# Kernel optimization log

Hardware: AMD Instinct MI355X
Metric: run time of the kernel (lower is better)

The kernel has to match this reference:

```python
import jax, jax.numpy as jnp
import numpy as np

X_GRID, Y_GRID = 192, 132
HW = X_GRID * Y_GRID            # 25344
NUM_PROP = 500
NUM_CLS = 6
RADIUS = 10
L_WIN = (2 * RADIUS + 1) ** 2   # 441
D = 128
N_HEADS = 8
D_HEAD = D // N_HEADS
VX, VY = 0.64, 0.64             # feature_map_stride * voxel_size
PC_X0, PC_Y0 = -61.44, -42.24


def _bev_pos():
    # create_2D_grid: linspace(0, size-1, size) + 0.5, meshgrid 'ij', flatten row-major
    bx, by = jnp.meshgrid(jnp.arange(X_GRID, dtype=jnp.float32) + 0.5,
                          jnp.arange(Y_GRID, dtype=jnp.float32) + 0.5, indexing='ij')
    return jnp.stack([bx.reshape(-1), by.reshape(-1)], axis=-1)[None]  # [1, HW, 2]


def conv2d(x, w, b):
    y = jax.lax.conv_general_dilated(x, w, (1, 1), 'SAME',
                                     dimension_numbers=('NCHW', 'OIHW', 'NCHW'))
    return y + b[None, :, None, None]


def maxpool3_valid(x):
    return jax.lax.reduce_window(x, -jnp.inf, jax.lax.max,
                                 (1, 1, 3, 3), (1, 1, 1, 1), 'VALID')


def layer_norm(x, g, b, eps=1e-5):
    m = jnp.mean(x, axis=-1, keepdims=True)
    v = jnp.var(x, axis=-1, keepdims=True)
    return (x - m) * jax.lax.rsqrt(v + eps) * g + b


def pos_emb(p, W1, b1, W2, b2):
    return jax.nn.relu(p @ W1 + b1) @ W2 + b2


def _forward(inputs, W_shared, b_shared, W_hm, b_hm, W_cls, b_cls,
             W_pos1, b_pos1, W_pos2, b_pos2, Wq, bq, Wk, bk, Wv, bv, Wo, bo,
             ln1_g, ln1_b, ln2_g, ln2_b, W_ff1, b_ff1, W_ff2, b_ff2,
             W_center, b_center, W_height, b_height, W_dim, b_dim,
             W_rot, b_rot, W_iou, b_iou, W_hm2, b_hm2):
    x = jnp.transpose(inputs, (0, 1, 3, 2))          # [B,C,192,132]
    B = x.shape[0]
    lidar_feat = jax.nn.relu(conv2d(x, W_shared, b_shared))   # [B,128,192,132]
    lff = lidar_feat.reshape(B, D, HW)

    dense_heatmap = conv2d(lidar_feat, W_hm, b_hm)            # [B,6,192,132]
    heatmap = jax.nn.sigmoid(jax.lax.stop_gradient(dense_heatmap))  # detached in original

    # local-max NMS: 3x3 maxpool on inner region, zeros at border; classes 3..5 bypass NMS
    inner = maxpool3_valid(heatmap)
    local_max = jnp.pad(inner, ((0, 0), (0, 0), (1, 1), (1, 1)))
    local_max = local_max.at[:, 3:6].set(heatmap[:, 3:6])
    hm = heatmap * (heatmap == local_max)

    # threshold + top-k proposals (replaces nonzero+pad+MySortImpe plugin)
    hm_flat = hm.reshape(B, NUM_CLS * HW)
    vals = jnp.where(hm_flat > 0.01, hm_flat, 0.0)
    _, top = jax.lax.top_k(vals, NUM_PROP)            # [B,500]
    cls = top // HW
    sp = top % HW

    query_feat = jnp.take_along_axis(lff, sp[:, None, :], axis=2)  # [B,128,500]
    oh = jax.nn.one_hot(cls, NUM_CLS, dtype=lff.dtype)             # [B,500,6]
    query_feat = query_feat + jnp.einsum('bpc,oc->bop', oh, W_cls) + b_cls[None, :, None]

    bev_pos = jnp.broadcast_to(_bev_pos(), (B, HW, 2))
    query_pos = jnp.take_along_axis(bev_pos, sp[:, :, None], axis=1)  # [B,500,2]

    # windowed key indices (faithful to original //x_grid, %y_grid arithmetic)
    rng = jnp.arange(-RADIUS, RADIUS + 1)
    rx, ry = jnp.meshgrid(rng, rng, indexing='ij')
    kx = (sp // X_GRID)[:, :, None, None] + rx[None, None]
    ky = (sp % Y_GRID)[:, :, None, None] + ry[None, None]
    key_idx = kx.reshape(B, NUM_PROP, L_WIN) * X_GRID + ky.reshape(B, NUM_PROP, L_WIN)
    key_mask = (key_idx < 0) | (key_idx >= HW)
    key_idx = jnp.clip(key_idx, 0, HW - 1)

    key_feat = jnp.take_along_axis(lff, key_idx.reshape(B, 1, -1), axis=2)
    key_feat = key_feat.reshape(B, D, NUM_PROP, L_WIN)
    key_pos = jnp.take_along_axis(bev_pos, key_idx.reshape(B, -1, 1), axis=1)
    key_pos = key_pos.reshape(B, NUM_PROP, L_WIN, 2)

    # decoder: cross-attention of each proposal over its 441-key window
    N = B * NUM_PROP
    q = query_feat.transpose(0, 2, 1).reshape(N, D)
    k = key_feat.transpose(0, 2, 3, 1).reshape(N, L_WIN, D)
    mask = key_mask.reshape(N, L_WIN)
    qpe = pos_emb(query_pos.reshape(N, 2), W_pos1, b_pos1, W_pos2, b_pos2)
    kpe = pos_emb(key_pos.reshape(N, L_WIN, 2), W_pos1, b_pos1, W_pos2, b_pos2)

    qh = ((q + qpe) @ Wq + bq).reshape(N, N_HEADS, D_HEAD)
    kh = ((k + kpe) @ Wk + bk).reshape(N, L_WIN, N_HEADS, D_HEAD)
    vh = (k @ Wv + bv).reshape(N, L_WIN, N_HEADS, D_HEAD)
    scores = jnp.einsum('nhd,nlhd->nhl', qh, kh) / np.float32(np.sqrt(D_HEAD))
    scores = jnp.where(mask[:, None, :], jnp.float32(-1e9), scores)
    attn = jax.nn.softmax(scores, axis=-1)
    ctx = jnp.einsum('nhl,nlhd->nhd', attn, vh).reshape(N, D)
    x1 = layer_norm(q + ctx @ Wo + bo, ln1_g, ln1_b)
    ff = jax.nn.relu(x1 @ W_ff1 + b_ff1) @ W_ff2 + b_ff2
    x2 = layer_norm(x1 + ff, ln2_g, ln2_b)

    qf = x2.reshape(B, NUM_PROP, D).transpose(0, 2, 1)   # [B,128,500]
    head = lambda W, b: jnp.einsum('bcp,oc->bop', qf, W) + b[None, :, None]
    center = head(W_center, b_center) + query_pos.transpose(0, 2, 1)
    height = head(W_height, b_height)
    dim = head(W_dim, b_dim)
    rot = head(W_rot, b_rot)
    iou = head(W_iou, b_iou)
    hm2 = head(W_hm2, b_hm2)

    # get_bboxes / decode_bbox
    score = jax.nn.sigmoid(hm2)                          # [B,6,500]
    _ = (iou + 1.0) * 0.5                                # computed, unused (as in original)
    final_preds = jnp.argmax(score, axis=1).astype(score.dtype)
    final_scores = jnp.max(score, axis=1)
    cx = center[:, 0:1] * VX + PC_X0
    cy = center[:, 1:2] * VY + PC_Y0
    dim = jnp.exp(dim)
    height = height - dim[:, 2:3] * 0.5
    rot = jnp.arctan(rot[:, 0:1] / (rot[:, 1:2] + 1e-6))
    box = jnp.concatenate([cx, cy, height, dim, rot,
                           final_preds[:, None, :], final_scores[:, None, :]], axis=1)
    return box.transpose(0, 2, 1)                        # [B,500,9]


def setup_inputs() -> dict:
    key = jax.random.key(0)
    ks = jax.random.split(key, 20)
    r = lambda k, shape, s=0.02: jax.random.normal(k, shape, dtype=jnp.float32) * s
    z = lambda n: jnp.zeros((n,), dtype=jnp.float32)
    o = lambda n: jnp.ones((n,), dtype=jnp.float32)
    return {
        'inputs': jax.random.normal(ks[0], (1, 256, 132, 192), dtype=jnp.float32),
        'W_shared': r(ks[1], (128, 256, 3, 3)), 'b_shared': z(128),
        'W_hm': r(ks[2], (6, 128, 3, 3)), 'b_hm': z(6),
        'W_cls': r(ks[3], (128, 6)), 'b_cls': z(128),
        'W_pos1': r(ks[4], (2, 128)), 'b_pos1': z(128),
        'W_pos2': r(ks[5], (128, 128)), 'b_pos2': z(128),
        'Wq': r(ks[6], (128, 128)), 'bq': z(128),
        'Wk': r(ks[7], (128, 128)), 'bk': z(128),
        'Wv': r(ks[8], (128, 128)), 'bv': z(128),
        'Wo': r(ks[9], (128, 128)), 'bo': z(128),
        'ln1_g': o(128), 'ln1_b': z(128),
        'ln2_g': o(128), 'ln2_b': z(128),
        'W_ff1': r(ks[10], (128, 256)), 'b_ff1': z(256),
        'W_ff2': r(ks[11], (256, 128)), 'b_ff2': z(128),
        'W_center': r(ks[12], (2, 128)), 'b_center': z(2),
        'W_height': r(ks[13], (1, 128)), 'b_height': z(1),
        'W_dim': r(ks[14], (3, 128)), 'b_dim': z(3),
        'W_rot': r(ks[15], (2, 128)), 'b_rot': z(2),
        'W_iou': r(ks[16], (1, 128)), 'b_iou': z(1),
        'W_hm2': r(ks[17], (6, 128)), 'b_hm2': z(6),
    }


def reference(inputs, W_shared, b_shared, W_hm, b_hm, W_cls, b_cls,
              W_pos1, b_pos1, W_pos2, b_pos2, Wq, bq, Wk, bk, Wv, bv, Wo, bo,
              ln1_g, ln1_b, ln2_g, ln2_b, W_ff1, b_ff1, W_ff2, b_ff2,
              W_center, b_center, W_height, b_height, W_dim, b_dim,
              W_rot, b_rot, W_iou, b_iou, W_hm2, b_hm2):
    return _forward(inputs, W_shared, b_shared, W_hm, b_hm, W_cls, b_cls,
                    W_pos1, b_pos1, W_pos2, b_pos2, Wq, bq, Wk, bk, Wv, bv, Wo, bo,
                    ln1_g, ln1_b, ln2_g, ln2_b, W_ff1, b_ff1, W_ff2, b_ff2,
                    W_center, b_center, W_height, b_height, W_dim, b_dim,
                    W_rot, b_rot, W_iou, b_iou, W_hm2, b_hm2)
```

## Files before the change

### kernel.cpp

```cpp
#include <hip/hip_runtime.h>
#include <math.h>
#include <float.h>

#define XG 192
#define YG 132
#define HW 25344
#define NCLS 6
#define NPROP 500
#define LWIN 441
#define CAP 2048

typedef unsigned short ushort_t;
typedef __attribute__((ext_vector_type(8))) short bf8v;
typedef __attribute__((ext_vector_type(4))) float f4v;

static __device__ __forceinline__ int imin(int a,int b){return a<b?a:b;}
static __device__ __forceinline__ int imax(int a,int b){return a>b?a:b;}

__device__ __forceinline__ void gl_lds16(const float* gp, float* lp){
  __builtin_amdgcn_global_load_lds(
      (const __attribute__((address_space(1))) unsigned int*)gp,
      (__attribute__((address_space(3))) unsigned int*)lp,
      16, 0, 0);
}
__device__ __forceinline__ void gl_lds16u(const ushort_t* gp, ushort_t* lp){
  __builtin_amdgcn_global_load_lds(
      (const __attribute__((address_space(1))) unsigned int*)gp,
      (__attribute__((address_space(3))) unsigned int*)lp,
      16, 0, 0);
}

__device__ __forceinline__ ushort_t f2bf(float x){
  unsigned u = __float_as_uint(x);
  return (ushort_t)((u + 0x7FFFu + ((u>>16)&1u)) >> 16);
}
__device__ __forceinline__ float bf2f(ushort_t h){
  return __uint_as_float(((unsigned)h)<<16);
}

__global__ __launch_bounds__(256) void k_wt(const float* __restrict__ Ws,
                                            const float* __restrict__ Whm,
                                            const float* __restrict__ Wq,
                                            const float* __restrict__ Wp2,
                                            const float* __restrict__ Wo,
                                            const float* __restrict__ Wf1,
                                            const float* __restrict__ Wf2,
                                            float* __restrict__ W6,
                                            float* __restrict__ WQT,
                                            float* __restrict__ WP2T,
                                            float* __restrict__ WOT,
                                            float* __restrict__ WF1T,
                                            float* __restrict__ WF2T,
                                            ushort_t* __restrict__ BQ0,
                                            ushort_t* __restrict__ BQ1,
                                            ushort_t* __restrict__ BQ2,
                                            int* __restrict__ Z){
  int t = blockIdx.x*256 + threadIdx.x;
  if (t < 294912){
    int kl = t & 31;
    int rest = t >> 5;
    int n = rest & 127;
    int tc = rest >> 7;
    int tap = tc >> 3, chunk = tc & 7;
    int c = chunk*32 + kl;
    float v = Ws[(size_t)n*2304 + c*9 + tap];
    ushort_t h0 = f2bf(v);
    float r1 = v - bf2f(h0);
    ushort_t h1 = f2bf(r1);
    float r2 = r1 - bf2f(h1);
    ushort_t h2 = f2bf(r2);
    size_t dst = (size_t)tc*5120 + n*40 + kl;
    BQ0[dst] = h0; BQ1[dst] = h1; BQ2[dst] = h2;
  }
  if (t < 6912){
    int c = t & 127, row = t >> 7;
    int cls = row / 9, tap = row % 9;
    W6[t] = Whm[(size_t)cls*1152 + c*9 + tap];
  }
  if (t < 16384){
    int k = t & 127, c = t >> 7;
    WQT[t]  = Wq [(size_t)k*128 + c];
    WP2T[t] = Wp2[(size_t)k*128 + c];
    WOT[t]  = Wo [(size_t)k*128 + c];
  }
  if (t < 32768){
    { int k = t & 127, o = t >> 7;  WF1T[t] = Wf1[(size_t)k*256 + o]; }
    { int k = t & 255, c = t >> 8;  WF2T[t] = Wf2[(size_t)k*128 + c]; }
  }
  if (t < 65568) Z[t] = 0;
}

__global__ __launch_bounds__(256, 3) void k_conv1(const float* __restrict__ IN,
                                                  const ushort_t* __restrict__ BQ0,
                                                  const ushort_t* __restrict__ BQ1,
                                                  const ushort_t* __restrict__ BQ2,
                                                  float* __restrict__ P0,
                                                  float* __restrict__ P1){
  const int b  = blockIdx.x;
  const int g  = blockIdx.y;
  const int i0 = (b % 3) * 64;
  const int j  = b / 3;
  const int tid = threadIdx.x;
  const int w    = tid >> 6;
  const int lane = tid & 63;
  const int l15  = lane & 15, quad = lane >> 4;
  __shared__ __align__(16) ushort_t SM[23280];
  ushort_t* As0 = SM;
  ushort_t* As1 = SM + 2640;
  ushort_t* As2 = SM + 5280;
  ushort_t* Bs0 = SM + 7920;
  ushort_t* Bs1 = SM + 13040;
  ushort_t* Bs2 = SM + 18160;
  f4v acc[4][2];
  #pragma unroll
  for (int mq=0;mq<4;++mq)
    #pragma unroll
    for (int nt=0;nt<2;++nt) acc[mq][nt] = (f4v){0.f,0.f,0.f,0.f};

  for (int cq=0; cq<4; ++cq){
    const int chunk = g*4 + cq;
    for (int kw=0; kw<3; ++kw){
      __syncthreads();
      {
        int gj = j - 1 + kw;
        bool jok = (unsigned)gj < 132u;
        for (int e = tid; e < 2112; e += 256){
          int c = e / 66, ii = e - c*66;
          int gi = i0 - 1 + ii;
          float v = 0.f;
          if (jok && (unsigned)gi < 192u)
            v = IN[(size_t)(chunk*32 + c)*25344 + gj*192 + gi];
          ushort_t h0 = f2bf(v);
          float r1 = v - bf2f(h0);
          ushort_t h1 = f2bf(r1);
          float r2 = r1 - bf2f(h1);
          ushort_t h2 = f2bf(r2);
          int a = ii*40 + c;
          As0[a] = h0; As1[a] = h1; As2[a] = h2;
        }
      }
      for (int kh=0; kh<3; ++kh){
        if (kh > 0) __syncthreads();
        {
          int tc = (kh*3 + kw)*8 + chunk;
          const ushort_t* s0 = BQ0 + (size_t)tc*5120;
          const ushort_t* s1 = BQ1 + (size_t)tc*5120;
          const ushort_t* s2 = BQ2 + (size_t)tc*5120;
          gl_lds16u(s0 + (size_t)tid*8,       Bs0 + (size_t)(w*64)*8);
          gl_lds16u(s0 + (size_t)(256+tid)*8, Bs0 + (size_t)(256 + w*64)*8);
          gl_lds16u(s1 + (size_t)tid*8,       Bs1 + (size_t)(w*64)*8);
          gl_lds16u(s1 + (size_t)(256+tid)*8, Bs1 + (size_t)(256 + w*64)*8);
          gl_lds16u(s2 + (size_t)tid*8,       Bs2 + (size_t)(w*64)*8);
          gl_lds16u(s2 + (size_t)(256+tid)*8, Bs2 + (size_t)(256 + w*64)*8);
          if (tid < 128){
            gl_lds16u(s0 + (size_t)(512+tid)*8, Bs0 + (size_t)(512 + w*64)*8);
            gl_lds16u(s1 + (size_t)(512+tid)*8, Bs1 + (size_t)(512 + w*64)*8);
            gl_lds16u(s2 + (size_t)(512+tid)*8, Bs2 + (size_t)(512 + w*64)*8);
          }
        }
        __syncthreads();
        bf8v A0[4], A1[4], A2[4];
        #pragma unroll
        for (int mq=0; mq<4; ++mq){
          int off = (mq*16 + l15 + kh)*40 + quad*8;
          A0[mq] = *(const bf8v*)&As0[off];
          A1[mq] = *(const bf8v*)&As1[off];
          A2[mq] = *(const bf8v*)&As2[off];
        }
        bf8v B0[2], B1[2], B2[2];
        #pragma unroll
        for (int ntl=0; ntl<2; ++ntl){
          int off = ((w*2+ntl)*16 + l15)*40 + quad*8;
          B0[ntl] = *(const bf8v*)&Bs0[off];
          B1[ntl] = *(const bf8v*)&Bs1[off];
          B2[ntl] = *(const bf8v*)&Bs2[off];
        }
        #pragma unroll
        for (int mq=0;mq<4;++mq){
          #pragma unroll
          for (int ntl=0;ntl<2;++ntl){
            f4v c = acc[mq][ntl];
            c = __builtin_amdgcn_mfma_f32_16x16x32_bf16(A0[mq], B0[ntl], c, 0,0,0);
            c = __builtin_amdgcn_mfma_f32_16x16x32_bf16(A0[mq], B1[ntl], c, 0,0,0);
            c = __builtin_amdgcn_mfma_f32_16x16x32_bf16(A1[mq], B0[ntl], c, 0,0,0);
            c = __builtin_amdgcn_mfma_f32_16x16x32_bf16(A0[mq], B2[ntl], c, 0,0,0);
            c = __builtin_amdgcn_mfma_f32_16x16x32_bf16(A1[mq], B1[ntl], c, 0,0,0);
            c = __builtin_amdgcn_mfma_f32_16x16x32_bf16(A2[mq], B0[ntl], c, 0,0,0);
            acc[mq][ntl] = c;
          }
        }
      }
    }
  }
  __syncthreads();
  float* Cs = (float*)SM;
  #pragma unroll
  for (int mq=0;mq<4;++mq)
    #pragma unroll
    for (int ntl=0;ntl<2;++ntl)
      #pragma unroll
      for (int r=0;r<4;++r){
        int m = mq*16 + quad*4 + r;
        int oc = (w*2+ntl)*16 + l15;
        Cs[m*128 + oc] = acc[mq][ntl][r];
      }
  __syncthreads();
  float* dst = g ? P1 : P0;
  for (int e = tid; e < 2048; e += 256){
    int m = e >> 5, ocq = e & 31;
    float4 v = *(float4*)&Cs[m*128 + ocq*4];
    int p = (i0 + m)*132 + j;
    *(float4*)&dst[(size_t)p*128 + ocq*4] = v;
  }
}

__global__ __launch_bounds__(256) void k_cadd2(float* __restrict__ LFF,
                                               const float* __restrict__ P0,
                                               const float* __restrict__ P1,
                                               const float* __restrict__ bias){
  int t = blockIdx.x*256 + threadIdx.x;
  float4 a = ((const float4*)P0)[t];
  float4 b = ((const float4*)P1)[t];
  float4 bs = ((const float4*)bias)[t & 31];
  float4 r;
  r.x = fmaxf(a.x+b.x+bs.x, 0.f);
  r.y = fmaxf(a.y+b.y+bs.y, 0.f);
  r.z = fmaxf(a.z+b.z+bs.z, 0.f);
  r.w = fmaxf(a.w+b.w+bs.w, 0.f);
  ((float4*)LFF)[t] = r;
}

__global__ __launch_bounds__(256) void k_mid(const float* __restrict__ LFF,
                                             const float* __restrict__ W1, const float* __restrict__ b1,
                                             const float* __restrict__ W2, const float* __restrict__ b2,
                                             const float* __restrict__ Wk, const float* __restrict__ bk,
                                             const float* __restrict__ Wv, const float* __restrict__ bv,
                                             float* __restrict__ KK, float* __restrict__ VV,
                                             const float* __restrict__ W6, const float* __restrict__ bhm,
                                             float* __restrict__ HMS){
  __shared__ float smem[12288];
  const int tid = threadIdx.x;
  const int wv4 = tid >> 6;
  if (blockIdx.x < 792){
    float* hs   = smem;
    float* sf   = smem + 4096;
    float* wbuf = smem + 8192;
    const int p0 = blockIdx.x*32;
    for (int e=tid; e<4096; e+=256){
      int k = e>>5, px = e&31;
      int p = p0+px;
      float bx = (float)(p/132)+0.5f, by = (float)(p%132)+0.5f;
      hs[k*32+px] = fmaxf(bx*W1[k] + by*W1[128+k] + b1[k], 0.f);
    }
    for (int e=tid; e<4096; e+=256){
      int px = e>>7, k = e&127;
      sf[k*32+px] = LFF[(size_t)(p0+px)*128 + k];
    }
    const int pxg = tid & 15, ocg = tid >> 4;
    const int px0 = pxg*2, oc0 = ocg*8;
    float accA[2][8];
    #pragma unroll
    for (int r=0;r<2;++r)
      #pragma unroll
      for (int u=0;u<8;++u) accA[r][u]=0.f;
    for (int c0=0; c0<128; c0+=32){
      __syncthreads();
      const float* wsrc = W2 + (size_t)c0*128;
      #pragma unroll
      for (int r=0;r<4;++r)
        gl_lds16(wsrc + (size_t)(r*256+tid)*4, wbuf + (size_t)(r*256+wv4*64)*4);
      __syncthreads();
      #pragma unroll 2
      for (int k=0;k<32;++k){
        float a0 = hs[(c0+k)*32+px0], a1 = hs[(c0+k)*32+px0+1];
        const float4* w = (const float4*)(wbuf + (size_t)k*128 + oc0);
        float4 w0 = w[0], w1 = w[1];
        accA[0][0]+=a0*w0.x; accA[0][1]+=a0*w0.y; accA[0][2]+=a0*w0.z; accA[0][3]+=a0*w0.w;
        accA[0][4]+=a0*w1.x; accA[0][5]+=a0*w1.y; accA[0][6]+=a0*w1.z; accA[0][7]+=a0*w1.w;
        accA[1][0]+=a1*w0.x; accA[1][1]+=a1*w0.y; accA[1][2]+=a1*w0.z; accA[1][3]+=a1*w0.w;
        accA[1][4]+=a1*w1.x; accA[1][5]+=a1*w1.y; accA[1][6]+=a1*w1.z; accA[1][7]+=a1*w1.w;
      }
    }
    __syncthreads();
    #pragma unroll
    for (int u=0;u<8;++u){
      float bb = b2[oc0+u];
      hs[(oc0+u)*32+px0]   = sf[(oc0+u)*32+px0]   + accA[0][u] + bb;
      hs[(oc0+u)*32+px0+1] = sf[(oc0+u)*32+px0+1] + accA[1][u] + bb;
    }
    float accK[2][8], accV[2][8];
    #pragma unroll
    for (int u=0;u<8;++u){
      float k0 = bk[oc0+u], v0 = bv[oc0+u];
      accK[0][u]=k0; accK[1][u]=k0; accV[0][u]=v0; accV[1][u]=v0;
    }
    for (int c0=0; c0<128; c0+=16){
      __syncthreads();
      #pragma unroll
      for (int r=0;r<2;++r){
        gl_lds16(Wk + (size_t)c0*128 + (size_t)(r*256+tid)*4, wbuf + (size_t)(r*256+wv4*64)*4);
        gl_lds16(Wv + (size_t)c0*128 + (size_t)(r*256+tid)*4, wbuf + 2048 + (size_t)(r*256+wv4*64)*4);
      }
      __syncthreads();
      #pragma unroll 2
      for (int k=0;k<16;++k){
        int kk = c0+k;
        float s0 = hs[kk*32+px0], s1 = hs[kk*32+px0+1];
        float f0 = sf[kk*32+px0], f1 = sf[kk*32+px0+1];
        const float4* wkp = (const float4*)(wbuf + (size_t)k*128 + oc0);
        const float4* wvp = (const float4*)(wbuf + 2048 + (size_t)k*128 + oc0);
        float4 k0v = wkp[0], k1v = wkp[1], v0v = wvp[0], v1v = wvp[1];
        accK[0][0]+=s0*k0v.x; accK[0][1]+=s0*k0v.y; accK[0][2]+=s0*k0v.z; accK[0][3]+=s0*k0v.w;
        accK[0][4]+=s0*k1v.x; accK[0][5]+=s0*k1v.y; accK[0][6]+=s0*k1v.z; accK[0][7]+=s0*k1v.w;
        accK[1][0]+=s1*k0v.x; accK[1][1]+=s1*k0v.y; accK[1][2]+=s1*k0v.z; accK[1][3]+=s1*k0v.w;
        accK[1][4]+=s1*k1v.x; accK[1][5]+=s1*k1v.y; accK[1][6]+=s1*k1v.z; accK[1][7]+=s1*k1v.w;
        accV[0][0]+=f0*v0v.x; accV[0][1]+=f0*v0v.y; accV[0][2]+=f0*v0v.z; accV[0][3]+=f0*v0v.w;
        accV[0][4]+=f0*v1v.x; accV[0][5]+=f0*v1v.y; accV[0][6]+=f0*v1v.z; accV[0][7]+=f0*v1v.w;
        accV[1][0]+=f1*v0v.x; accV[1][1]+=f1*v0v.y; accV[1][2]+=f1*v0v.z; accV[1][3]+=f1*v0v.w;
        accV[1][4]+=f1*v1v.x; accV[1][5]+=f1*v1v.y; accV[1][6]+=f1*v1v.z; accV[1][7]+=f1*v1v.w;
      }
    }
    #pragma unroll
    for (int r=0;r<2;++r){
      int p = p0+px0+r;
      float4* oK = (float4*)(KK + (size_t)p*128 + oc0);
      float4* oV = (float4*)(VV + (size_t)p*128 + oc0);
      float4 t0, t1;
      t0.x=accK[r][0]; t0.y=accK[r][1]; t0.z=accK[r][2]; t0.w=accK[r][3];
      t1.x=accK[r][4]; t1.y=accK[r][5]; t1.z=accK[r][6]; t1.w=accK[r][7];
      oK[0]=t0; oK[1]=t1;
      t0.x=accV[r][0]; t0.y=accV[r][1]; t0.z=accV[r][2]; t0.w=accV[r][3];
      t1.x=accV[r][4]; t1.y=accV[r][5]; t1.z=accV[r][6]; t1.w=accV[r][7];
      oV[0]=t0; oV[1]=t1;
    }
  } else {
    float* w6s = smem;
    float* red = smem + 8192;
    for (int e=tid; e<6912; e+=256) w6s[e] = W6[e];
    __syncthreads();
    int lane = tid & 63, wave = tid >> 6;
    int p = (blockIdx.x - 792)*64 + lane;
    int i = p/132, j = p%132;
    float acc[6] = {0.f,0.f,0.f,0.f,0.f,0.f};
    int cbase = wave*32;
    #pragma unroll
    for (int kh=0; kh<3; ++kh){
      int gi = i+kh-1;
      if ((unsigned)gi >= 192u) continue;
      #pragma unroll
      for (int kw=0; kw<3; ++kw){
        int gj = j+kw-1;
        if ((unsigned)gj >= 132u) continue;
        const float* row = LFF + (size_t)(gi*132+gj)*128 + cbase;
        int tap = kh*3+kw;
        #pragma unroll
        for (int cq=0; cq<8; ++cq){
          float4 v = *(const float4*)(row + cq*4);
          #pragma unroll
          for (int cls=0; cls<6; ++cls){
            float4 wv = *(const float4*)(w6s + (size_t)(cls*9+tap)*128 + cbase + cq*4);
            acc[cls] += v.x*wv.x + v.y*wv.y + v.z*wv.z + v.w*wv.w;
          }
        }
      }
    }
    __syncthreads();
    #pragma unroll
    for (int c=0;c<6;++c) red[(wave*6+c)*64 + lane] = acc[c];
    __syncthreads();
    if (wave==0){
      #pragma unroll
      for (int c=0;c<6;++c){
        float s = red[c*64+lane] + red[(6+c)*64+lane] + red[(12+c)*64+lane] + red[(18+c)*64+lane] + bhm[c];
        HMS[(size_t)c*HW + p] = 1.f/(1.f+expf(-s));
      }
    }
  }
}

__global__ __launch_bounds__(256) void k_nms(const float* __restrict__ HMS,
                                             float* __restrict__ VALS,
                                             int* __restrict__ HIST){
  int t = blockIdx.x*256 + threadIdx.x;
  int c = t / HW, p = t % HW;
  int i = p/132, j = p%132;
  float h = HMS[t];
  float v;
  if (c < 3){
    v = 0.f;
    if (i>=1 && i<=190 && j>=1 && j<=130){
      float m = -1e30f;
      #pragma unroll
      for (int di=-1;di<=1;++di)
        #pragma unroll
        for (int dj=-1;dj<=1;++dj)
          m = fmaxf(m, HMS[(size_t)c*HW + (i+di)*132 + (j+dj)]);
      if (h == m) v = h;
    }
  } else v = h;
  if (!(v > 0.01f)) v = 0.f;
  VALS[t] = v;
  if (v > 0.f) atomicAdd(HIST + (__float_as_uint(v)>>16), 1);
}

__global__ __launch_bounds__(1024) void k_scan(const int* __restrict__ HIST, int* __restrict__ SCAN){
  __shared__ int part[1024];
  __shared__ int gsel;
  int t = threadIdx.x;
  int s = 0, base = t*64;
  for (int u=0;u<64;++u) s += HIST[base+u];
  part[t] = s;
  __syncthreads();
  for (int off=1; off<1024; off<<=1){
    int add = (t+off < 1024) ? part[t+off] : 0;
    __syncthreads();
    part[t] += add;
    __syncthreads();
  }
  int total = part[0];
  int mineI = part[t];
  int nextI = (t < 1023) ? part[t+1] : 0;
  if (mineI >= NPROP && nextI < NPROP) gsel = t;
  if (t == 0 && total < NPROP) gsel = -1;
  __syncthreads();
  int g = gsel;
  if (g < 0){
    if (t==0){ SCAN[0] = 0; SCAN[1] = total; }
    return;
  }
  int cumG = (g < 1023) ? part[g+1] : 0;
  if (t < 64){
    int x = HIST[g*64 + t];
    #pragma unroll
    for (int off=1; off<64; off<<=1){
      int y = __shfl_down(x, off);
      x += (t + off < 64) ? y : 0;
    }
    int Snext = __shfl_down(x, 1);
    int incl  = cumG + x;
    int nextc = (t==63) ? cumG : cumG + Snext;
    if (incl >= NPROP && nextc < NPROP){
      SCAN[0] = g*64 + t;
      SCAN[1] = nextc;
    }
  }
}

__global__ __launch_bounds__(256) void k_collect(const float* __restrict__ VALS,
                                                 const int* __restrict__ SCAN,
                                                 int* __restrict__ CNT,
                                                 float* __restrict__ CV, int* __restrict__ CI){
  int t = blockIdx.x*256 + threadIdx.x;
  float v = VALS[t];
  int bstar = SCAN[0];
  if (v > 0.f && (int)(__float_as_uint(v)>>16) >= bstar){
    int pos = atomicAdd(CNT, 1);
    if (pos < CAP){ CV[pos] = v; CI[pos] = t; }
  }
}

__global__ __launch_bounds__(1024) void k_sort(const float* __restrict__ CV, const int* __restrict__ CI,
                                               const int* __restrict__ CNT,
                                               int* __restrict__ TOPS, int* __restrict__ TOPC){
  __shared__ float sv[CAP];
  __shared__ int   si[CAP];
  int tid = threadIdx.x;
  int M = imin(CNT[0], CAP);
  for (int i=tid; i<CAP; i+=1024){
    if (i < M){ sv[i] = CV[i]; si[i] = CI[i]; }
    else      { sv[i] = -1.f;  si[i] = 0x7fffffff; }
  }
  __syncthreads();
  for (int k=2; k<=CAP; k<<=1){
    for (int j=k>>1; j>0; j>>=1){
      for (int i=tid; i<CAP; i+=1024){
        int p = i ^ j;
        if (p > i){
          bool up = ((i & k) == 0);
          float va = sv[i], vb = sv[p];
          int ia = si[i], ib = si[p];
          bool aFirst = (va > vb) || (va == vb && ia < ib);
          bool bFirst = (vb > va) || (vb == va && ib < ia);
          bool doswap = up ? bFirst : aFirst;
          if (doswap){ sv[i]=vb; sv[p]=va; si[i]=ib; si[p]=ia; }
        }
      }
      __syncthreads();
    }
  }
  for (int t=tid; t<NPROP; t+=1024){
    int idx = imin(si[t], NCLS*HW - 1);
    TOPC[t] = idx / HW;
    TOPS[t] = idx % HW;
  }
}

__global__ __launch_bounds__(256) void k_attn(const float* __restrict__ KK, const float* __restrict__ VV,
                                              const float* __restrict__ LFF,
                                              const int* __restrict__ TOPS, const int* __restrict__ TOPC,
                                              const float* __restrict__ Wcls, const float* __restrict__ bcls,
                                              const float* __restrict__ pW1, const float* __restrict__ pb1,
                                              const float* __restrict__ WP2T, const float* __restrict__ pb2,
                                              const float* __restrict__ WQT, const float* __restrict__ bq,
                                              const float* __restrict__ WOT, const float* __restrict__ bo,
                                              const float* __restrict__ g1, const float* __restrict__ b1,
                                              const float* __restrict__ WF1T, const float* __restrict__ bf1,
                                              const float* __restrict__ WF2T, const float* __restrict__ bf2,
                                              const float* __restrict__ g2, const float* __restrict__ b2,
                                              const float* __restrict__ Wc, const float* __restrict__ bc,
                                              const float* __restrict__ Wh, const float* __restrict__ bh,
                                              const float* __restrict__ Wd, const float* __restrict__ bd,
                                              const float* __restrict__ Wr, const float* __restrict__ br,
                                              const float* __restrict__ Whm2, const float* __restrict__ bhm2,
                                              float* __restrict__ out){
  int n = blockIdx.x, tid = threadIdx.x;
  __shared__ __align__(16) float qhL[128];
  __shared__ float sc[8*441];
  __shared__ int   kiL[441];
  __shared__ __align__(16) float ctxL[128];
  __shared__ float xL[128];
  __shared__ float hidL[256];
  __shared__ float sumsL[8];
  __shared__ float stat[2];
  __shared__ float dots[16];
  int sp = TOPS[n];
  int cls = TOPC[n];
  const int kb64 = (tid>>7)*64, c128 = tid&127;
  float qreg = 0.f;
  if (tid < 128){
    float qx = (float)(sp/132)+0.5f, qy = (float)(sp%132)+0.5f;
    ctxL[tid] = fmaxf(qx*pW1[tid] + qy*pW1[128+tid] + pb1[tid], 0.f);
    qreg = LFF[(size_t)sp*128+tid] + Wcls[tid*6+cls] + bcls[tid];
  }
  __syncthreads();
  {
    const float4* wp = (const float4*)(WP2T + (size_t)c128*128 + kb64);
    float pe = 0.f;
    #pragma unroll
    for (int k4=0;k4<16;++k4){
      float4 w = wp[k4]; int kb = kb64 + k4*4;
      pe += ctxL[kb]*w.x + ctxL[kb+1]*w.y + ctxL[kb+2]*w.z + ctxL[kb+3]*w.w;
    }
    sc[tid] = pe;
  }
  __syncthreads();
  if (tid < 128) xL[tid] = qreg + pb2[tid] + sc[tid] + sc[tid+128];
  __syncthreads();
  {
    const float4* wp = (const float4*)(WQT + (size_t)c128*128 + kb64);
    float qh = 0.f;
    #pragma unroll
    for (int k4=0;k4<16;++k4){
      float4 w = wp[k4]; int kb = kb64 + k4*4;
      qh += xL[kb]*w.x + xL[kb+1]*w.y + xL[kb+2]*w.z + xL[kb+3]*w.w;
    }
    sc[tid] = qh;
  }
  __syncthreads();
  if (tid < 128) qhL[tid] = bq[tid] + sc[tid] + sc[tid+128];
  __syncthreads();
  int spx = sp/192, spy = sp%132;
  for (int l = tid; l < 441; l += 256){
    int a = l/21, bb = l%21;
    int kidx = (spx + a - 10)*192 + (spy + bb - 10);
    bool msk = (kidx < 0) || (kidx >= HW);
    int kc = imin(imax(kidx,0), HW-1);
    kiL[l] = kc;
    const float4* kk4 = (const float4*)(KK + (size_t)kc*128);
    const float4* qh4 = (const float4*)qhL;
    #pragma unroll
    for (int hh=0; hh<8; ++hh){
      float acc = 0.f;
      #pragma unroll
      for (int d4=0; d4<4; ++d4){
        float4 kv = kk4[hh*4+d4]; float4 qv = qh4[hh*4+d4];
        acc += kv.x*qv.x + kv.y*qv.y + kv.z*qv.z + kv.w*qv.w;
      }
      sc[hh*441+l] = msk ? -1e9f : acc*0.25f;
    }
  }
  __syncthreads();
  int wave = tid>>6, lane = tid&63;
  for (int hh = wave; hh < 8; hh += 4){
    float mx = -3.0e38f;
    for (int l = lane; l < 441; l += 64) mx = fmaxf(mx, sc[hh*441+l]);
    #pragma unroll
    for (int off=32; off; off>>=1) mx = fmaxf(mx, __shfl_xor(mx, off));
    float sum = 0.f;
    for (int l = lane; l < 441; l += 64){
      float e = __expf(sc[hh*441+l] - mx);
      sc[hh*441+l] = e; sum += e;
    }
    #pragma unroll
    for (int off=32; off; off>>=1) sum += __shfl_xor(sum, off);
    if (lane==0) sumsL[hh] = sum;
  }
  __syncthreads();
  for (int hh = wave; hh < 8; hh += 4){
    float a[16];
    #pragma unroll
    for (int d=0; d<16; ++d) a[d]=0.f;
    for (int l = lane; l < 441; l += 64){
      float w = sc[hh*441+l];
      const float4* vv4 = (const float4*)(VV + (size_t)kiL[l]*128 + hh*16);
      #pragma unroll
      for (int d4=0; d4<4; ++d4){
        float4 v = vv4[d4];
        a[d4*4+0]+=w*v.x; a[d4*4+1]+=w*v.y; a[d4*4+2]+=w*v.z; a[d4*4+3]+=w*v.w;
      }
    }
    #pragma unroll
    for (int d=0; d<16; ++d){
      #pragma unroll
      for (int off=32; off; off>>=1) a[d] += __shfl_xor(a[d], off);
    }
    if (lane==0){
      float inv = 1.f/sumsL[hh];
      #pragma unroll
      for (int d=0; d<16; ++d) ctxL[hh*16+d] = a[d]*inv;
    }
  }
  __syncthreads();
  {
    const float4* wp = (const float4*)(WOT + (size_t)c128*128 + kb64);
    float acc = 0.f;
    #pragma unroll
    for (int k4=0;k4<16;++k4){
      float4 w = wp[k4]; int kb = kb64 + k4*4;
      acc += ctxL[kb]*w.x + ctxL[kb+1]*w.y + ctxL[kb+2]*w.z + ctxL[kb+3]*w.w;
    }
    sc[tid] = acc;
  }
  __syncthreads();
  float x1v = 0.f;
  if (tid < 128){
    x1v = qreg + bo[tid] + sc[tid] + sc[tid+128];
    xL[tid] = x1v;
  }
  __syncthreads();
  if (tid < 64){
    float u0 = xL[tid], u1 = xL[tid+64];
    float s = u0+u1, s2 = u0*u0+u1*u1;
    #pragma unroll
    for (int off=32; off; off>>=1){ s += __shfl_xor(s, off); s2 += __shfl_xor(s2, off); }
    if (tid==0){ float mean = s*(1.f/128.f); float var = s2*(1.f/128.f) - mean*mean;
      stat[0]=mean; stat[1]=rsqrtf(var + 1e-5f); }
  }
  __syncthreads();
  if (tid < 128) xL[tid] = (x1v - stat[0])*stat[1]*g1[tid] + b1[tid];
  __syncthreads();
  {
    const float4* wp = (const float4*)(WF1T + (size_t)tid*128);
    float hv = bf1[tid];
    #pragma unroll 8
    for (int k4=0;k4<32;++k4){
      float4 w = wp[k4]; int kb = k4*4;
      hv += xL[kb]*w.x + xL[kb+1]*w.y + xL[kb+2]*w.z + xL[kb+3]*w.w;
    }
    hidL[tid] = fmaxf(hv, 0.f);
  }
  __syncthreads();
  {
    int kb0 = (tid>>7)*128;
    const float4* wp = (const float4*)(WF2T + (size_t)c128*256 + kb0);
    float acc = 0.f;
    #pragma unroll 8
    for (int k4=0;k4<32;++k4){
      float4 w = wp[k4]; int kb = kb0 + k4*4;
      acc += hidL[kb]*w.x + hidL[kb+1]*w.y + hidL[kb+2]*w.z + hidL[kb+3]*w.w;
    }
    sc[tid] = acc;
  }
  __syncthreads();
  float x2v = 0.f;
  if (tid < 128) x2v = xL[tid] + bf2[tid] + sc[tid] + sc[tid+128];
  __syncthreads();
  if (tid < 128) hidL[tid] = x2v;
  __syncthreads();
  if (tid < 64){
    float u0 = hidL[tid], u1 = hidL[tid+64];
    float s = u0+u1, s2 = u0*u0+u1*u1;
    #pragma unroll
    for (int off=32; off; off>>=1){ s += __shfl_xor(s, off); s2 += __shfl_xor(s2, off); }
    if (tid==0){ float mean = s*(1.f/128.f); float var = s2*(1.f/128.f) - mean*mean;
      stat[0]=mean; stat[1]=rsqrtf(var + 1e-5f); }
  }
  __syncthreads();
  if (tid < 128) xL[tid] = (x2v - stat[0])*stat[1]*g2[tid] + b2[tid];
  __syncthreads();
  if (tid < 14){
    const float* Wp; float bb;
    if (tid < 2)      { Wp = Wc + tid*128;        bb = bc[tid];      }
    else if (tid < 3) { Wp = Wh;                  bb = bh[0];        }
    else if (tid < 6) { Wp = Wd + (tid-3)*128;    bb = bd[tid-3];    }
    else if (tid < 8) { Wp = Wr + (tid-6)*128;    bb = br[tid-6];    }
    else              { Wp = Whm2 + (tid-8)*128;  bb = bhm2[tid-8];  }
    float acc = bb;
    for (int k=0;k<128;++k) acc += xL[k]*Wp[k];
    dots[tid] = acc;
  }
  __syncthreads();
  if (tid == 0){
    float qpx = (float)(sp/132)+0.5f, qpy = (float)(sp%132)+0.5f;
    float cx = (dots[0]+qpx)*0.64f - 61.44f;
    float cy = (dots[1]+qpy)*0.64f - 42.24f;
    float e0 = expf(dots[3]), e1 = expf(dots[4]), e2 = expf(dots[5]);
    float hgt = dots[2] - e2*0.5f;
    float rot = atanf(dots[6]/(dots[7] + 1e-6f));
    float bestv = -1.f; int bestc = 0;
    #pragma unroll
    for (int m=0;m<6;++m){
      float s = 1.f/(1.f + expf(-dots[8+m]));
      if (s > bestv){ bestv = s; bestc = m; }
    }
    float* o = out + (size_t)n*9;
    o[0]=cx; o[1]=cy; o[2]=hgt; o[3]=e0; o[4]=e1; o[5]=e2; o[6]=rot;
    o[7]=(float)bestc; o[8]=bestv;
  }
}

extern "C" void kernel_launch(void* const* d_in, const int* in_sizes, int n_in,
                              void* d_out, int out_size, void* d_ws, size_t ws_size,
                              hipStream_t stream){
  (void)in_sizes; (void)n_in; (void)out_size;
  const float* IN   = (const float*)d_in[0];
  const float* Wsh  = (const float*)d_in[1];
  const float* bsh  = (const float*)d_in[2];
  const float* Whm  = (const float*)d_in[3];
  const float* bhm  = (const float*)d_in[4];
  const float* Wcls = (const float*)d_in[5];
  const float* bcls = (const float*)d_in[6];
  const float* Wp1  = (const float*)d_in[7];
  const float* bp1  = (const float*)d_in[8];
  const float* Wp2  = (const float*)d_in[9];
  const float* bp2  = (const float*)d_in[10];
  const float* Wq   = (const float*)d_in[11];
  const float* bq   = (const float*)d_in[12];
  const float* Wk   = (const float*)d_in[13];
  const float* bk   = (const float*)d_in[14];
  const float* Wv   = (const float*)d_in[15];
  const float* bv   = (const float*)d_in[16];
  const float* Wo   = (const float*)d_in[17];
  const float* bo   = (const float*)d_in[18];
  const float* g1   = (const float*)d_in[19];
  const float* b1   = (const float*)d_in[20];
  const float* g2   = (const float*)d_in[21];
  const float* b2   = (const float*)d_in[22];
  const float* Wf1  = (const float*)d_in[23];
  const float* bf1  = (const float*)d_in[24];
  const float* Wf2  = (const float*)d_in[25];
  const float* bf2  = (const float*)d_in[26];
  const float* Wc   = (const float*)d_in[27];
  const float* bc   = (const float*)d_in[28];
  const float* Wh   = (const float*)d_in[29];
  const float* bh   = (const float*)d_in[30];
  const float* Wd   = (const float*)d_in[31];
  const float* bd   = (const float*)d_in[32];
  const float* Wr   = (const float*)d_in[33];
  const float* br   = (const float*)d_in[34];
  const float* Whm2 = (const float*)d_in[37];
  const float* bhm2 = (const float*)d_in[38];
  float* out = (float*)d_out;
  float* W = (float*)d_ws;

  const size_t N_LFF  = (size_t)HW*128;
  const size_t OFF_LFF  = 0;
  const size_t OFF_KK   = OFF_LFF + N_LFF;
  const size_t OFF_VV   = OFF_KK + N_LFF;
  const size_t OFF_W6   = OFF_VV + N_LFF;
  const size_t OFF_HMS  = OFF_W6 + 6912;
  const size_t OFF_VALS = OFF_HMS + 152064;
  const size_t OFF_HIST = OFF_VALS + 152064;
  const size_t OFF_SCAN = OFF_HIST + 65536;
  const size_t OFF_CNT  = OFF_SCAN + 16;
  const size_t OFF_CV   = OFF_CNT + 16;
  const size_t OFF_CI   = OFF_CV + CAP;
  const size_t OFF_TOPS = OFF_CI + CAP;
  const size_t OFF_TOPC = OFF_TOPS + 512;
  const size_t OFF_WQT  = OFF_TOPC + 512;
  const size_t OFF_WP2T = OFF_WQT + 16384;
  const size_t OFF_WOT  = OFF_WP2T + 16384;
  const size_t OFF_WF1T = OFF_WOT + 16384;
  const size_t OFF_WF2T = OFF_WF1T + 32768;
  const size_t OFF_BQ0  = OFF_WF2T + 32768;
  const size_t OFF_BQ1  = OFF_BQ0 + 184320;
  const size_t OFF_BQ2  = OFF_BQ1 + 184320;
  const size_t TOTAL    = OFF_BQ2 + 184320;
  if (ws_size < TOTAL*sizeof(float)) return;

  ushort_t* BQ0 = (ushort_t*)(W + OFF_BQ0);
  ushort_t* BQ1 = (ushort_t*)(W + OFF_BQ1);
  ushort_t* BQ2 = (ushort_t*)(W + OFF_BQ2);

  k_wt    <<<1152, 256, 0, stream>>>(Wsh, Whm, Wq, Wp2, Wo, Wf1, Wf2,
                                     W+OFF_W6,
                                     W+OFF_WQT, W+OFF_WP2T, W+OFF_WOT, W+OFF_WF1T, W+OFF_WF2T,
                                     BQ0, BQ1, BQ2,
                                     (int*)(W+OFF_HIST));
  k_conv1 <<<dim3(396,2), 256, 0, stream>>>(IN, BQ0, BQ1, BQ2, W+OFF_KK, W+OFF_VV);
  k_cadd2 <<<3168, 256, 0, stream>>>(W+OFF_LFF, W+OFF_KK, W+OFF_VV, bsh);
  k_mid   <<<1188, 256, 0, stream>>>(W+OFF_LFF, Wp1, bp1, Wp2, bp2, Wk, bk, Wv, bv,
                                     W+OFF_KK, W+OFF_VV, W+OFF_W6, bhm, W+OFF_HMS);
  k_nms   <<<594,  256, 0, stream>>>(W+OFF_HMS, W+OFF_VALS, (int*)(W+OFF_HIST));
  k_scan  <<<1,   1024, 0, stream>>>((const int*)(W+OFF_HIST), (int*)(W+OFF_SCAN));
  k_collect<<<594, 256, 0, stream>>>(W+OFF_VALS, (const int*)(W+OFF_SCAN),
                                     (int*)(W+OFF_CNT), W+OFF_CV, (int*)(W+OFF_CI));
  k_sort  <<<1,   1024, 0, stream>>>(W+OFF_CV, (const int*)(W+OFF_CI), (const int*)(W+OFF_CNT),
                                     (int*)(W+OFF_TOPS), (int*)(W+OFF_TOPC));
  k_attn  <<<500,  256, 0, stream>>>(W+OFF_KK, W+OFF_VV, W+OFF_LFF,
                                     (const int*)(W+OFF_TOPS), (const int*)(W+OFF_TOPC),
                                     Wcls, bcls, Wp1, bp1, W+OFF_WP2T, bp2, W+OFF_WQT, bq,
                                     W+OFF_WOT, bo, g1, b1, W+OFF_WF1T, bf1, W+OFF_WF2T, bf2, g2, b2,
                                     Wc, bc, Wh, bh, Wd, bd, Wr, br, Whm2, bhm2, out);
}
```

Before: 541.7 us.

## Enlarge conv1 tile to 96 rows and stage input via LDS transpose

The shared 3x3 conv kernel now covers 96 rows per block instead of 64, cutting the grid from 396x2 to 264x2 blocks. Each B weight tile loaded into LDS is therefore reused across six M-tiles instead of four. Input loading is split into a coalesced raw fp32 load into a padded LDS buffer, followed by a transposed pass that splits values into three bf16 parts. The extra LDS, more accumulators and the lower occupancy hint (2 blocks per SM instead of 3) reduce occupancy and add a sync per kw step.

```diff
diff --git a/kernel.cpp b/kernel.cpp
--- a/kernel.cpp
+++ b/kernel.cpp
@@ -90,7 +90,7 @@
   if (t < 65568) Z[t] = 0;
 }
 
-__global__ __launch_bounds__(256, 3) void k_conv1(const float* __restrict__ IN,
+__global__ __launch_bounds__(256, 2) void k_conv1(const float* __restrict__ IN,
                                                   const ushort_t* __restrict__ BQ0,
                                                   const ushort_t* __restrict__ BQ1,
                                                   const ushort_t* __restrict__ BQ2,
@@ -98,22 +98,23 @@
                                                   float* __restrict__ P1){
   const int b  = blockIdx.x;
   const int g  = blockIdx.y;
-  const int i0 = (b % 3) * 64;
-  const int j  = b / 3;
+  const int i0 = (b & 1) * 96;
+  const int j  = b >> 1;
   const int tid = threadIdx.x;
   const int w    = tid >> 6;
   const int lane = tid & 63;
   const int l15  = lane & 15, quad = lane >> 4;
-  __shared__ __align__(16) ushort_t SM[23280];
+  __shared__ __align__(16) ushort_t SM[33584];
   ushort_t* As0 = SM;
-  ushort_t* As1 = SM + 2640;
-  ushort_t* As2 = SM + 5280;
-  ushort_t* Bs0 = SM + 7920;
-  ushort_t* Bs1 = SM + 13040;
-  ushort_t* Bs2 = SM + 18160;
-  f4v acc[4][2];
+  ushort_t* As1 = SM + 3920;
+  ushort_t* As2 = SM + 7840;
+  ushort_t* Bs0 = SM + 11760;
+  ushort_t* Bs1 = SM + 16880;
+  ushort_t* Bs2 = SM + 22000;
+  float*    araw = (float*)(SM + 27120);
+  f4v acc[6][2];
   #pragma unroll
-  for (int mq=0;mq<4;++mq)
+  for (int mq=0;mq<6;++mq)
     #pragma unroll
     for (int nt=0;nt<2;++nt) acc[mq][nt] = (f4v){0.f,0.f,0.f,0.f};
 
@@ -124,20 +125,26 @@
       {
         int gj = j - 1 + kw;
         bool jok = (unsigned)gj < 132u;
-        for (int e = tid; e < 2112; e += 256){
-          int c = e / 66, ii = e - c*66;
+        for (int e = tid; e < 3136; e += 256){
+          int c = e / 98, ii = e - c*98;
           int gi = i0 - 1 + ii;
           float v = 0.f;
           if (jok && (unsigned)gi < 192u)
             v = IN[(size_t)(chunk*32 + c)*25344 + gj*192 + gi];
-          ushort_t h0 = f2bf(v);
-          float r1 = v - bf2f(h0);
-          ushort_t h1 = f2bf(r1);
-          float r2 = r1 - bf2f(h1);
-          ushort_t h2 = f2bf(r2);
-          int a = ii*40 + c;
-          As0[a] = h0; As1[a] = h1; As2[a] = h2;
+          araw[c*101 + ii] = v;
         }
+      }
+      __syncthreads();
+      for (int e = tid; e < 3136; e += 256){
+        int c = e & 31, ii = e >> 5;
+        float v = araw[c*101 + ii];
+        ushort_t h0 = f2bf(v);
+        float r1 = v - bf2f(h0);
+        ushort_t h1 = f2bf(r1);
+        float r2 = r1 - bf2f(h1);
+        ushort_t h2 = f2bf(r2);
+        int a = ii*40 + c;
+        As0[a] = h0; As1[a] = h1; As2[a] = h2;
       }
       for (int kh=0; kh<3; ++kh){
         if (kh > 0) __syncthreads();
@@ -159,14 +166,6 @@
           }
         }
         __syncthreads();
-        bf8v A0[4], A1[4], A2[4];
-        #pragma unroll
-        for (int mq=0; mq<4; ++mq){
-          int off = (mq*16 + l15 + kh)*40 + quad*8;
-          A0[mq] = *(const bf8v*)&As0[off];
-          A1[mq] = *(const bf8v*)&As1[off];
-          A2[mq] = *(const bf8v*)&As2[off];
-        }
         bf8v B0[2], B1[2], B2[2];
         #pragma unroll
         for (int ntl=0; ntl<2; ++ntl){
@@ -176,16 +175,20 @@
           B2[ntl] = *(const bf8v*)&Bs2[off];
         }
         #pragma unroll
-        for (int mq=0;mq<4;++mq){
+        for (int mq=0;mq<6;++mq){
+          int offA = (mq*16 + l15 + kh)*40 + quad*8;
+          bf8v A0 = *(const bf8v*)&As0[offA];
+          bf8v A1 = *(const bf8v*)&As1[offA];
+          bf8v A2 = *(const bf8v*)&As2[offA];
           #pragma unroll
           for (int ntl=0;ntl<2;++ntl){
             f4v c = acc[mq][ntl];
-            c = __builtin_amdgcn_mfma_f32_16x16x32_bf16(A0[mq], B0[ntl], c, 0,0,0);
-            c = __builtin_amdgcn_mfma_f32_16x16x32_bf16(A0[mq], B1[ntl], c, 0,0,0);
-            c = __builtin_amdgcn_mfma_f32_16x16x32_bf16(A1[mq], B0[ntl], c, 0,0,0);
-            c = __builtin_amdgcn_mfma_f32_16x16x32_bf16(A0[mq], B2[ntl], c, 0,0,0);
-            c = __builtin_amdgcn_mfma_f32_16x16x32_bf16(A1[mq], B1[ntl], c, 0,0,0);
-            c = __builtin_amdgcn_mfma_f32_16x16x32_bf16(A2[mq], B0[ntl], c, 0,0,0);
+            c = __builtin_amdgcn_mfma_f32_16x16x32_bf16(A0, B0[ntl], c, 0,0,0);
+            c = __builtin_amdgcn_mfma_f32_16x16x32_bf16(A0, B1[ntl], c, 0,0,0);
+            c = __builtin_amdgcn_mfma_f32_16x16x32_bf16(A1, B0[ntl], c, 0,0,0);
+            c = __builtin_amdgcn_mfma_f32_16x16x32_bf16(A0, B2[ntl], c, 0,0,0);
+            c = __builtin_amdgcn_mfma_f32_16x16x32_bf16(A1, B1[ntl], c, 0,0,0);
+            c = __builtin_amdgcn_mfma_f32_16x16x32_bf16(A2, B0[ntl], c, 0,0,0);
             acc[mq][ntl] = c;
           }
         }
@@ -195,7 +198,7 @@
   __syncthreads();
   float* Cs = (float*)SM;
   #pragma unroll
-  for (int mq=0;mq<4;++mq)
+  for (int mq=0;mq<6;++mq)
     #pragma unroll
     for (int ntl=0;ntl<2;++ntl)
       #pragma unroll
@@ -206,7 +209,7 @@
       }
   __syncthreads();
   float* dst = g ? P1 : P0;
-  for (int e = tid; e < 2048; e += 256){
+  for (int e = tid; e < 3072; e += 256){
     int m = e >> 5, ocq = e & 31;
     float4 v = *(float4*)&Cs[m*128 + ocq*4];
     int p = (i0 + m)*132 + j;
@@ -797,7 +800,7 @@
                                      W+OFF_WQT, W+OFF_WP2T, W+OFF_WOT, W+OFF_WF1T, W+OFF_WF2T,
                                      BQ0, BQ1, BQ2,
                                      (int*)(W+OFF_HIST));
-  k_conv1 <<<dim3(396,2), 256, 0, stream>>>(IN, BQ0, BQ1, BQ2, W+OFF_KK, W+OFF_VV);
+  k_conv1 <<<dim3(264,2), 256, 0, stream>>>(IN, BQ0, BQ1, BQ2, W+OFF_KK, W+OFF_VV);
   k_cadd2 <<<3168, 256, 0, stream>>>(W+OFF_LFF, W+OFF_KK, W+OFF_VV, bsh);
   k_mid   <<<1188, 256, 0, stream>>>(W+OFF_LFF, Wp1, bp1, Wp2, bp2, Wk, bk, Wv, bv,
                                      W+OFF_KK, W+OFF_VV, W+OFF_W6, bhm, W+OFF_HMS);
```

New measurement: 591.3 us. 1.09x slower.

## Sort proposals spatially and widen attention blocks to 512 threads

Applied to the files above, without the earlier changes.

After the top-k bitonic sort, the 500 proposals are re-sorted by spatial index so that neighbouring blocks fetch overlapping key/value windows. Block IDs are interleaved across XCDs, and a rank array maps results back to their original output rows. The attention kernel goes from 256 to 512 threads: each of the 8 waves takes one head, and the matvecs split K four ways. This aims at better L2 reuse of the K/V gathers and more parallelism per proposal, at the cost of an extra sort, more LDS partial-sum reductions, and lower occupancy per block.

```diff
diff --git a/kernel.cpp b/kernel.cpp
--- a/kernel.cpp
+++ b/kernel.cpp
@@ -461,9 +461,12 @@
 
 __global__ __launch_bounds__(1024) void k_sort(const float* __restrict__ CV, const int* __restrict__ CI,
                                                const int* __restrict__ CNT,
-                                               int* __restrict__ TOPS, int* __restrict__ TOPC){
+                                               int* __restrict__ TOPS, int* __restrict__ TOPC,
+                                               int* __restrict__ RANK){
   __shared__ float sv[CAP];
   __shared__ int   si[CAP];
+  __shared__ int   keyA[512];
+  __shared__ int   clsA[512];
   int tid = threadIdx.x;
   int M = imin(CNT[0], CAP);
   for (int i=tid; i<CAP; i+=1024){
@@ -488,16 +491,41 @@
       __syncthreads();
     }
   }
-  for (int t=tid; t<NPROP; t+=1024){
-    int idx = imin(si[t], NCLS*HW - 1);
-    TOPC[t] = idx / HW;
-    TOPS[t] = idx % HW;
-  }
-}
-
-__global__ __launch_bounds__(256) void k_attn(const float* __restrict__ KK, const float* __restrict__ VV,
+  if (tid < 512){
+    if (tid < NPROP){
+      int idx = imin(si[tid], NCLS*HW - 1);
+      keyA[tid] = (idx % HW)*512 + tid;
+      clsA[tid] = idx / HW;
+    } else { keyA[tid] = 0x7fffffff; clsA[tid] = 0; }
+  }
+  __syncthreads();
+  for (int k=2; k<=512; k<<=1){
+    for (int j=k>>1; j>0; j>>=1){
+      if (tid < 512){
+        int i = tid, p = i ^ j;
+        if (p > i){
+          bool up = ((i & k) == 0);
+          int ka = keyA[i], kb = keyA[p];
+          bool doswap = up ? (ka > kb) : (ka < kb);
+          if (doswap){ keyA[i]=kb; keyA[p]=ka; }
+        }
+      }
+      __syncthreads();
+    }
+  }
+  if (tid < 512){
+    int k = keyA[tid];
+    int r = k & 511;
+    TOPS[tid] = k >> 9;
+    TOPC[tid] = clsA[r];
+    RANK[tid] = r;
+  }
+}
+
+__global__ __launch_bounds__(512) void k_attn(const float* __restrict__ KK, const float* __restrict__ VV,
                                               const float* __restrict__ LFF,
                                               const int* __restrict__ TOPS, const int* __restrict__ TOPC,
+                                              const int* __restrict__ RANK,
                                               const float* __restrict__ Wcls, const float* __restrict__ bcls,
                                               const float* __restrict__ pW1, const float* __restrict__ pb1,
                                               const float* __restrict__ WP2T, const float* __restrict__ pb2,
@@ -513,7 +541,10 @@
                                               const float* __restrict__ Wr, const float* __restrict__ br,
                                               const float* __restrict__ Whm2, const float* __restrict__ bhm2,
                                               float* __restrict__ out){
-  int n = blockIdx.x, tid = threadIdx.x;
+  int bx = blockIdx.x;
+  int n = (bx & 7)*64 + (bx >> 3);
+  if (n >= NPROP) return;
+  int tid = threadIdx.x;
   __shared__ __align__(16) float qhL[128];
   __shared__ float sc[8*441];
   __shared__ int   kiL[441];
@@ -525,7 +556,8 @@
   __shared__ float dots[16];
   int sp = TOPS[n];
   int cls = TOPC[n];
-  const int kb64 = (tid>>7)*64, c128 = tid&127;
+  int orow = RANK[n];
+  const int c128 = tid & 127, ks4 = (tid >> 7) * 32;
   float qreg = 0.f;
   if (tid < 128){
     float qx = (float)(sp/132)+0.5f, qy = (float)(sp%132)+0.5f;
@@ -534,33 +566,33 @@
   }
   __syncthreads();
   {
-    const float4* wp = (const float4*)(WP2T + (size_t)c128*128 + kb64);
+    const float4* wp = (const float4*)(WP2T + (size_t)c128*128 + ks4);
     float pe = 0.f;
     #pragma unroll
-    for (int k4=0;k4<16;++k4){
-      float4 w = wp[k4]; int kb = kb64 + k4*4;
+    for (int k4=0;k4<8;++k4){
+      float4 w = wp[k4]; int kb = ks4 + k4*4;
       pe += ctxL[kb]*w.x + ctxL[kb+1]*w.y + ctxL[kb+2]*w.z + ctxL[kb+3]*w.w;
     }
     sc[tid] = pe;
   }
   __syncthreads();
-  if (tid < 128) xL[tid] = qreg + pb2[tid] + sc[tid] + sc[tid+128];
+  if (tid < 128) xL[tid] = qreg + pb2[tid] + ((sc[tid] + sc[tid+128]) + (sc[tid+256] + sc[tid+384]));
   __syncthreads();
   {
-    const float4* wp = (const float4*)(WQT + (size_t)c128*128 + kb64);
+    const float4* wp = (const float4*)(WQT + (size_t)c128*128 + ks4);
     float qh = 0.f;
     #pragma unroll
-    for (int k4=0;k4<16;++k4){
-      float4 w = wp[k4]; int kb = kb64 + k4*4;
+    for (int k4=0;k4<8;++k4){
+      float4 w = wp[k4]; int kb = ks4 + k4*4;
       qh += xL[kb]*w.x + xL[kb+1]*w.y + xL[kb+2]*w.z + xL[kb+3]*w.w;
     }
     sc[tid] = qh;
   }
   __syncthreads();
-  if (tid < 128) qhL[tid] = bq[tid] + sc[tid] + sc[tid+128];
+  if (tid < 128) qhL[tid] = bq[tid] + ((sc[tid] + sc[tid+128]) + (sc[tid+256] + sc[tid+384]));
   __syncthreads();
   int spx = sp/192, spy = sp%132;
-  for (int l = tid; l < 441; l += 256){
+  for (int l = tid; l < 441; l += 512){
     int a = l/21, bb = l%21;
     int kidx = (spx + a - 10)*192 + (spy + bb - 10);
     bool msk = (kidx < 0) || (kidx >= HW);
@@ -581,7 +613,8 @@
   }
   __syncthreads();
   int wave = tid>>6, lane = tid&63;
-  for (int hh = wave; hh < 8; hh += 4){
+  {
+    int hh = wave;
     float mx = -3.0e38f;
     for (int l = lane; l < 441; l += 64) mx = fmaxf(mx, sc[hh*441+l]);
     #pragma unroll
@@ -596,7 +629,8 @@
     if (lane==0) sumsL[hh] = sum;
   }
   __syncthreads();
-  for (int hh = wave; hh < 8; hh += 4){
+  {
+    int hh = wave;
     float a[16];
     #pragma unroll
     for (int d=0; d<16; ++d) a[d]=0.f;
@@ -622,11 +656,11 @@
   }
   __syncthreads();
   {
-    const float4* wp = (const float4*)(WOT + (size_t)c128*128 + kb64);
+    const float4* wp = (const float4*)(WOT + (size_t)c128*128 + ks4);
     float acc = 0.f;
     #pragma unroll
-    for (int k4=0;k4<16;++k4){
-      float4 w = wp[k4]; int kb = kb64 + k4*4;
+    for (int k4=0;k4<8;++k4){
+      float4 w = wp[k4]; int kb = ks4 + k4*4;
       acc += ctxL[kb]*w.x + ctxL[kb+1]*w.y + ctxL[kb+2]*w.z + ctxL[kb+3]*w.w;
     }
     sc[tid] = acc;
@@ -634,7 +668,7 @@
   __syncthreads();
   float x1v = 0.f;
   if (tid < 128){
-    x1v = qreg + bo[tid] + sc[tid] + sc[tid+128];
+    x1v = qreg + bo[tid] + ((sc[tid] + sc[tid+128]) + (sc[tid+256] + sc[tid+384]));
     xL[tid] = x1v;
   }
   __syncthreads();
@@ -650,30 +684,33 @@
   if (tid < 128) xL[tid] = (x1v - stat[0])*stat[1]*g1[tid] + b1[tid];
   __syncthreads();
   {
-    const float4* wp = (const float4*)(WF1T + (size_t)tid*128);
-    float hv = bf1[tid];
-    #pragma unroll 8
-    for (int k4=0;k4<32;++k4){
-      float4 w = wp[k4]; int kb = k4*4;
+    int o = tid & 255, half = tid >> 8;
+    const float4* wp = (const float4*)(WF1T + (size_t)o*128 + half*64);
+    float hv = 0.f;
+    #pragma unroll
+    for (int k4=0;k4<16;++k4){
+      float4 w = wp[k4]; int kb = half*64 + k4*4;
       hv += xL[kb]*w.x + xL[kb+1]*w.y + xL[kb+2]*w.z + xL[kb+3]*w.w;
     }
-    hidL[tid] = fmaxf(hv, 0.f);
-  }
+    sc[tid] = hv;
+  }
+  __syncthreads();
+  if (tid < 256) hidL[tid] = fmaxf(bf1[tid] + sc[tid] + sc[tid+256], 0.f);
   __syncthreads();
   {
-    int kb0 = (tid>>7)*128;
-    const float4* wp = (const float4*)(WF2T + (size_t)c128*256 + kb0);
+    int q = tid >> 7;
+    const float4* wp = (const float4*)(WF2T + (size_t)c128*256 + q*64);
     float acc = 0.f;
-    #pragma unroll 8
-    for (int k4=0;k4<32;++k4){
-      float4 w = wp[k4]; int kb = kb0 + k4*4;
+    #pragma unroll
+    for (int k4=0;k4<16;++k4){
+      float4 w = wp[k4]; int kb = q*64 + k4*4;
       acc += hidL[kb]*w.x + hidL[kb+1]*w.y + hidL[kb+2]*w.z + hidL[kb+3]*w.w;
     }
     sc[tid] = acc;
   }
   __syncthreads();
   float x2v = 0.f;
-  if (tid < 128) x2v = xL[tid] + bf2[tid] + sc[tid] + sc[tid+128];
+  if (tid < 128) x2v = xL[tid] + bf2[tid] + ((sc[tid] + sc[tid+128]) + (sc[tid+256] + sc[tid+384]));
   __syncthreads();
   if (tid < 128) hidL[tid] = x2v;
   __syncthreads();
@@ -713,7 +750,7 @@
       float s = 1.f/(1.f + expf(-dots[8+m]));
       if (s > bestv){ bestv = s; bestc = m; }
     }
-    float* o = out + (size_t)n*9;
+    float* o = out + (size_t)orow*9;
     o[0]=cx; o[1]=cy; o[2]=hgt; o[3]=e0; o[4]=e1; o[5]=e2; o[6]=rot;
     o[7]=(float)bestc; o[8]=bestv;
   }
@@ -777,7 +814,8 @@
   const size_t OFF_CI   = OFF_CV + CAP;
   const size_t OFF_TOPS = OFF_CI + CAP;
   const size_t OFF_TOPC = OFF_TOPS + 512;
-  const size_t OFF_WQT  = OFF_TOPC + 512;
+  const size_t OFF_RANK = OFF_TOPC + 512;
+  const size_t OFF_WQT  = OFF_RANK + 512;
   const size_t OFF_WP2T = OFF_WQT + 16384;
   const size_t OFF_WOT  = OFF_WP2T + 16384;
   const size_t OFF_WF1T = OFF_WOT + 16384;
@@ -806,9 +844,10 @@
   k_collect<<<594, 256, 0, stream>>>(W+OFF_VALS, (const int*)(W+OFF_SCAN),
                                      (int*)(W+OFF_CNT), W+OFF_CV, (int*)(W+OFF_CI));
   k_sort  <<<1,   1024, 0, stream>>>(W+OFF_CV, (const int*)(W+OFF_CI), (const int*)(W+OFF_CNT),
-                                     (int*)(W+OFF_TOPS), (int*)(W+OFF_TOPC));
-  k_attn  <<<500,  256, 0, stream>>>(W+OFF_KK, W+OFF_VV, W+OFF_LFF,
+                                     (int*)(W+OFF_TOPS), (int*)(W+OFF_TOPC), (int*)(W+OFF_RANK));
+  k_attn  <<<512,  512, 0, stream>>>(W+OFF_KK, W+OFF_VV, W+OFF_LFF,
                                      (const int*)(W+OFF_TOPS), (const int*)(W+OFF_TOPC),
+                                     (const int*)(W+OFF_RANK),
                                      Wcls, bcls, Wp1, bp1, W+OFF_WP2T, bp2, W+OFF_WQT, bq,
                                      W+OFF_WOT, bo, g1, b1, W+OFF_WF1T, bf1, W+OFF_WF2T, bf2, g2, b2,
                                      Wc, bc, Wh, bh, Wd, bd, Wr, br, Whm2, bhm2, out);
```

Measured after the change: 549.2 us. Within noise of the previous version (+1.4%).
